# Kernel tuning notes

Hardware: AMD Instinct MI355X
Metric: run time of the kernel (lower is better)

## Reference

```python
import jax, jax.numpy as jnp
import numpy as np

N_STU, N_ITEM, N_CONC = 10000, 50000, 2048
EDGES, K = 250000, 4
EMB, CNUM = 64, 128


def setup_inputs() -> dict:
    key = jax.random.key(0)
    ks = jax.random.split(key, 10)
    return {
        "stu_idx": jax.random.randint(ks[0], (EDGES,), 0, N_STU),
        "item_idx": jax.random.randint(ks[1], (EDGES,), 0, N_ITEM),
        "conc_idx": jax.random.randint(ks[2], (EDGES, K), 0, N_CONC),
        "stu_fusion": jax.random.normal(ks[3], (N_STU, EMB), jnp.float32),
        "item_fusion": jax.random.normal(ks[4], (N_ITEM, EMB), jnp.float32),
        "concept_fusion": jax.random.normal(ks[5], (N_CONC, EMB), jnp.float32),
        # factor weights are non-negative in the original (NoneNegClipper)
        "W_stu": jax.random.uniform(ks[6], (CNUM, 2 * EMB), jnp.float32) * 0.1,
        "W_item": jax.random.uniform(ks[7], (CNUM, 2 * EMB), jnp.float32) * 0.1,
        "w_pred": jax.random.uniform(ks[8], (CNUM,), jnp.float32) * 0.1,
        "b_pred": jax.random.normal(ks[9], (1,), jnp.float32),
    }


def reference(stu_idx, item_idx, conc_idx, stu_fusion, item_fusion,
              concept_fusion, W_stu, W_item, w_pred, b_pred):
    emb = stu_fusion.shape[1]
    # split Linear(2*emb -> CNUM) into the two cat halves: out = x1 @ Wa.T + x2 @ Wb.T
    Ws_a, Ws_b = W_stu[:, :emb], W_stu[:, emb:]
    Wi_a, Wi_b = W_item[:, :emb], W_item[:, emb:]

    # per-entity projections computed once on the tables, then gathered (cheap)
    stu_part = (stu_fusion @ Ws_a.T)[stu_idx]      # [E, CNUM]
    item_part = (item_fusion @ Wi_a.T)[item_idx]   # [E, CNUM]
    conc_stu = (concept_fusion @ Ws_b.T)[conc_idx]   # [E, K, CNUM]
    conc_item = (concept_fusion @ Wi_b.T)[conc_idx]  # [E, K, CNUM]

    stu_out = jax.nn.sigmoid(stu_part[:, None, :] + conc_stu)    # [E, K, CNUM]
    item_out = jax.nn.sigmoid(item_part[:, None, :] + conc_item)  # [E, K, CNUM]
    diff = stu_out - item_out
    per_conc = jax.nn.sigmoid(jnp.einsum('ekc,c->ek', diff, w_pred) + b_pred[0])  # [E, K]
    return per_conc.mean(axis=1)  # [E]
```

## Files before the change

kernel.cpp:

```cpp
#include <hip/hip_runtime.h>
#include <hip/hip_bf16.h>
#include <hip/hip_fp16.h>

constexpr int EDGES = 250000;
constexpr int EMB   = 64;
constexpr int CNUM  = 128;
constexpr int NSTU  = 10000;
constexpr int NITEM = 50000;
constexpr int NCONC = 2048;

constexpr size_t ESP_OFF = 0;
constexpr size_t EIP_OFF = ESP_OFF + (size_t)NSTU  * CNUM;
constexpr size_t ECS_OFF = EIP_OFF + (size_t)NITEM * CNUM;
constexpr size_t ECI_OFF = ECS_OFF + (size_t)NCONC * CNUM;

constexpr int TILE = 16;
constexpr int STU_TILES   = NSTU  / TILE;
constexpr int ITEM_TILES  = NITEM / TILE;
constexpr int CONC_GROUPS = (NCONC / TILE)*2;
constexpr int TOTAL_BLKS  = STU_TILES + ITEM_TILES + CONC_GROUPS;

constexpr float NEG_LOG2E = -1.44269504088896340736f;

__global__ __launch_bounds__(256) void proj_all(
        const float* __restrict__ stuF, const float* __restrict__ itemF,
        const float* __restrict__ concF,
        const float* __restrict__ W_stu, const float* __restrict__ W_item,
        __half* __restrict__ ESP, __half* __restrict__ EIP,
        __half* __restrict__ ECS, __half* __restrict__ ECI) {
    __shared__ float fs[TILE * EMB];
    const int b    = blockIdx.x;
    const int tid  = threadIdx.x;
    const int wv   = tid >> 6;
    const int lane = tid & 63;
    const int cl   = lane & 31;
    const int kh   = lane >> 5;
    const int c    = wv * 32 + cl;

    const float* F; const float* W; __half* O; int row0, wcol;
    if (b < STU_TILES) {
        F = stuF;  W = W_stu;  O = ESP; row0 = b * TILE; wcol = 0;
    } else if (b < STU_TILES + ITEM_TILES) {
        F = itemF; W = W_item; O = EIP; row0 = (b - STU_TILES) * TILE; wcol = 0;
    } else {
        const int g = b - STU_TILES - ITEM_TILES;
        F = concF; W = (g & 1) ? W_item : W_stu; O = (g & 1) ? ECI : ECS;
        row0 = (g >> 1) * TILE; wcol = EMB;
    }

    ((float4*)fs)[tid] = ((const float4*)(F + (size_t)row0 * EMB))[tid];

    float w[32];
    const float4* Wr = (const float4*)(W + c * (2 * EMB) + wcol + kh * 32);
#pragma unroll
    for (int j = 0; j < 8; ++j) {
        float4 u = Wr[j];
        w[4*j+0] = u.x; w[4*j+1] = u.y; w[4*j+2] = u.z; w[4*j+3] = u.w;
    }
    __syncthreads();

#pragma unroll
    for (int r = 0; r < TILE; ++r) {
        const float4* fr = (const float4*)(fs + r * EMB + kh * 32);
        float a0 = 0.f, a1 = 0.f, a2 = 0.f, a3 = 0.f;
#pragma unroll
        for (int j = 0; j < 8; ++j) {
            float4 u = fr[j];
            a0 = fmaf(u.x, w[4*j+0], a0);
            a1 = fmaf(u.y, w[4*j+1], a1);
            a2 = fmaf(u.z, w[4*j+2], a2);
            a3 = fmaf(u.w, w[4*j+3], a3);
        }
        float d = (a0 + a1) + (a2 + a3);
        d += __shfl_xor(d, 32, 64);
        const float e = __builtin_amdgcn_exp2f(d * NEG_LOG2E);
        if (kh == 0) O[(size_t)(row0 + r) * CNUM + c] = __float2half(e);
    }
}

__device__ __forceinline__ void h8f(const uint4 u, float* f) {
    const __half2* h = (const __half2*)&u;
#pragma unroll
    for (int i = 0; i < 4; ++i) {
        float2 v = __half22float2(h[i]);
        f[2*i] = v.x; f[2*i+1] = v.y;
    }
}

__device__ __forceinline__ float chan(float es, float ec, float ei, float ecc,
                                      float w) {
    const float t = es * ec;
    const float u = ei * ecc;
    return (w * (u - t)) * __builtin_amdgcn_rcpf((1.f + t) * (1.f + u));
}

__device__ __forceinline__ float sigm(float x) {
    return __builtin_amdgcn_rcpf(1.f + __builtin_amdgcn_exp2f(x * NEG_LOG2E));
}

__global__ __launch_bounds__(256) void edge_kernel(
        const int*  __restrict__ stu_idx,
        const int*  __restrict__ item_idx,
        const int4* __restrict__ conc_idx,
        const __half* __restrict__ ESP,
        const __half* __restrict__ EIP,
        const __half* __restrict__ ECS,
        const __half* __restrict__ ECI,
        const float* __restrict__ w_pred,
        const float* __restrict__ b_pred,
        float* __restrict__ out) {
    const int lane = threadIdx.x & 63;
    const int wvg  = (blockIdx.x * blockDim.x + threadIdx.x) >> 6;
    const int sub  = lane >> 4;
    const int li   = lane & 15;
    const int e    = wvg * 4 + sub;

    const int s  = stu_idx[e];
    const int it = item_idx[e];
    const int4 c4 = conc_idx[e];

    float es[8], ei[8], wf[8];
    h8f(*(const uint4*)(ESP + (size_t)s  * CNUM + li * 8), es);
    h8f(*(const uint4*)(EIP + (size_t)it * CNUM + li * 8), ei);
    {
        const float4* wp4 = (const float4*)(w_pred + li * 8);
        float4 a = wp4[0], b4 = wp4[1];
        wf[0]=a.x; wf[1]=a.y; wf[2]=a.z; wf[3]=a.w;
        wf[4]=b4.x; wf[5]=b4.y; wf[6]=b4.z; wf[7]=b4.w;
    }
    const float b = b_pred[0];

    const int ck[4] = {c4.x, c4.y, c4.z, c4.w};
    float p[4];
#pragma unroll
    for (int k = 0; k < 4; ++k) {
        float cs[8], ci[8];
        h8f(*(const uint4*)(ECS + (size_t)ck[k] * CNUM + li * 8), cs);
        h8f(*(const uint4*)(ECI + (size_t)ck[k] * CNUM + li * 8), ci);
        float a0 = 0.f, a1 = 0.f;
#pragma unroll
        for (int j = 0; j < 8; j += 2) {
            a0 += chan(es[j],   cs[j],   ei[j],   ci[j],   wf[j]);
            a1 += chan(es[j+1], cs[j+1], ei[j+1], ci[j+1], wf[j+1]);
        }
        p[k] = a0 + a1;
    }

#pragma unroll
    for (int m = 1; m <= 8; m <<= 1) {
        p[0] += __shfl_xor(p[0], m, 64);
        p[1] += __shfl_xor(p[1], m, 64);
        p[2] += __shfl_xor(p[2], m, 64);
        p[3] += __shfl_xor(p[3], m, 64);
    }

    const float r = 0.25f * (sigm(p[0] + b) + sigm(p[1] + b) +
                             sigm(p[2] + b) + sigm(p[3] + b));
    if (li == 0) out[e] = r;
}

extern "C" void kernel_launch(void* const* d_in, const int* in_sizes, int n_in,
                              void* d_out, int out_size, void* d_ws, size_t ws_size,
                              hipStream_t stream) {
    const int* stu_idx  = (const int*)d_in[0];
    const int* item_idx = (const int*)d_in[1];
    const int* conc_idx = (const int*)d_in[2];
    const float* stu_fusion     = (const float*)d_in[3];
    const float* item_fusion    = (const float*)d_in[4];
    const float* concept_fusion = (const float*)d_in[5];
    const float* W_stu          = (const float*)d_in[6];
    const float* W_item         = (const float*)d_in[7];
    const float* w_pred         = (const float*)d_in[8];
    const float* b_pred         = (const float*)d_in[9];
    float* out = (float*)d_out;

    __half* ESP = (__half*)d_ws + ESP_OFF;
    __half* EIP = (__half*)d_ws + EIP_OFF;
    __half* ECS = (__half*)d_ws + ECS_OFF;
    __half* ECI = (__half*)d_ws + ECI_OFF;

    proj_all<<<TOTAL_BLKS, 256, 0, stream>>>(
        stu_fusion, item_fusion, concept_fusion, W_stu, W_item,
        ESP, EIP, ECS, ECI);

    edge_kernel<<<EDGES / 16, 256, 0, stream>>>(
        stu_idx, item_idx, (const int4*)conc_idx,
        ESP, EIP, ECS, ECI, w_pred, b_pred, out);
}
```

Measured before the change: 150.8 us.

## Compute table projections with fp16 MFMA, one 16-row strip per wavefront

Replaces the scalar-FMA projection kernel with a per-wavefront MFMA 16x16x32 fp16 matrix multiply. Each wave handles one 16-row strip across all 128 channels, converting the fp32 features and weights to fp16 in registers. The goal is to cut the ALU-bound projection cost and the LDS staging. In exchange it adds fp16 rounding of inputs before accumulation, and the weights are reloaded from global memory by every wave.

```diff
diff --git a/kernel.cpp b/kernel.cpp
--- a/kernel.cpp
+++ b/kernel.cpp
@@ -14,67 +14,77 @@
 constexpr size_t ECS_OFF = EIP_OFF + (size_t)NITEM * CNUM;
 constexpr size_t ECI_OFF = ECS_OFF + (size_t)NCONC * CNUM;
 
-constexpr int TILE = 16;
-constexpr int STU_TILES   = NSTU  / TILE;
-constexpr int ITEM_TILES  = NITEM / TILE;
-constexpr int CONC_GROUPS = (NCONC / TILE)*2;
-constexpr int TOTAL_BLKS  = STU_TILES + ITEM_TILES + CONC_GROUPS;
-
 constexpr float NEG_LOG2E = -1.44269504088896340736f;
 
-__global__ __launch_bounds__(256) void proj_all(
+constexpr int STU_JOBS  = NSTU  / 16;
+constexpr int ITEM_JOBS = NITEM / 16;
+constexpr int CONC_JOBS = (NCONC / 16) * 2;
+constexpr int NJOBS     = STU_JOBS + ITEM_JOBS + CONC_JOBS;
+constexpr int PROJ_BLKS = (NJOBS + 3) / 4;
+
+typedef _Float16 half8 __attribute__((ext_vector_type(8)));
+typedef float    f32x4 __attribute__((ext_vector_type(4)));
+
+__device__ __forceinline__ half8 pack8(float4 lo, float4 hi) {
+    half8 h;
+    h[0] = (_Float16)lo.x; h[1] = (_Float16)lo.y;
+    h[2] = (_Float16)lo.z; h[3] = (_Float16)lo.w;
+    h[4] = (_Float16)hi.x; h[5] = (_Float16)hi.y;
+    h[6] = (_Float16)hi.z; h[7] = (_Float16)hi.w;
+    return h;
+}
+
+__global__ __launch_bounds__(256) void proj_mfma(
         const float* __restrict__ stuF, const float* __restrict__ itemF,
         const float* __restrict__ concF,
         const float* __restrict__ W_stu, const float* __restrict__ W_item,
         __half* __restrict__ ESP, __half* __restrict__ EIP,
         __half* __restrict__ ECS, __half* __restrict__ ECI) {
-    __shared__ float fs[TILE * EMB];
-    const int b    = blockIdx.x;
     const int tid  = threadIdx.x;
-    const int wv   = tid >> 6;
     const int lane = tid & 63;
-    const int cl   = lane & 31;
-    const int kh   = lane >> 5;
-    const int c    = wv * 32 + cl;
+    const int job  = blockIdx.x * 4 + (tid >> 6);
+    if (job >= NJOBS) return;
 
-    const float* F; const float* W; __half* O; int row0, wcol;
-    if (b < STU_TILES) {
-        F = stuF;  W = W_stu;  O = ESP; row0 = b * TILE; wcol = 0;
-    } else if (b < STU_TILES + ITEM_TILES) {
-        F = itemF; W = W_item; O = EIP; row0 = (b - STU_TILES) * TILE; wcol = 0;
+    const float* F; const float* W; __half* O; int strip, wcol;
+    if (job < STU_JOBS) {
+        F = stuF;  W = W_stu;  O = ESP; strip = job; wcol = 0;
+    } else if (job < STU_JOBS + ITEM_JOBS) {
+        F = itemF; W = W_item; O = EIP; strip = job - STU_JOBS; wcol = 0;
     } else {
-        const int g = b - STU_TILES - ITEM_TILES;
+        const int g = job - STU_JOBS - ITEM_JOBS;
         F = concF; W = (g & 1) ? W_item : W_stu; O = (g & 1) ? ECI : ECS;
-        row0 = (g >> 1) * TILE; wcol = EMB;
+        strip = g >> 1; wcol = EMB;
     }
 
-    ((float4*)fs)[tid] = ((const float4*)(F + (size_t)row0 * EMB))[tid];
+    const int m = lane & 15;
+    const int q = lane >> 4;
+    const int row = strip * 16 + m;
 
-    float w[32];
-    const float4* Wr = (const float4*)(W + c * (2 * EMB) + wcol + kh * 32);
-#pragma unroll
-    for (int j = 0; j < 8; ++j) {
-        float4 u = Wr[j];
-        w[4*j+0] = u.x; w[4*j+1] = u.y; w[4*j+2] = u.z; w[4*j+3] = u.w;
-    }
-    __syncthreads();
+    const float4* fa = (const float4*)(F + (size_t)row * EMB + q * 8);
+    const float4* fb = (const float4*)(F + (size_t)row * EMB + 32 + q * 8);
+    const half8 A0 = pack8(fa[0], fa[1]);
+    const half8 A1 = pack8(fb[0], fb[1]);
+
+    const int orow = strip * 16 + q * 4;
 
 #pragma unroll
-    for (int r = 0; r < TILE; ++r) {
-        const float4* fr = (const float4*)(fs + r * EMB + kh * 32);
-        float a0 = 0.f, a1 = 0.f, a2 = 0.f, a3 = 0.f;
+    for (int ct = 0; ct < 8; ++ct) {
+        const int ch = ct * 16 + m;
+        const float* wr = W + (size_t)ch * (2 * EMB) + wcol;
+        const float4* wb0 = (const float4*)(wr + q * 8);
+        const float4* wb1 = (const float4*)(wr + 32 + q * 8);
+        const half8 B0 = pack8(wb0[0], wb0[1]);
+        const half8 B1 = pack8(wb1[0], wb1[1]);
+
+        f32x4 acc = {0.f, 0.f, 0.f, 0.f};
+        acc = __builtin_amdgcn_mfma_f32_16x16x32_f16(A0, B0, acc, 0, 0, 0);
+        acc = __builtin_amdgcn_mfma_f32_16x16x32_f16(A1, B1, acc, 0, 0, 0);
+
 #pragma unroll
-        for (int j = 0; j < 8; ++j) {
-            float4 u = fr[j];
-            a0 = fmaf(u.x, w[4*j+0], a0);
-            a1 = fmaf(u.y, w[4*j+1], a1);
-            a2 = fmaf(u.z, w[4*j+2], a2);
-            a3 = fmaf(u.w, w[4*j+3], a3);
+        for (int r = 0; r < 4; ++r) {
+            const float e = __builtin_amdgcn_exp2f(acc[r] * NEG_LOG2E);
+            O[(size_t)(orow + r) * CNUM + ct * 16 + m] = __float2half(e);
         }
-        float d = (a0 + a1) + (a2 + a3);
-        d += __shfl_xor(d, 32, 64);
-        const float e = __builtin_amdgcn_exp2f(d * NEG_LOG2E);
-        if (kh == 0) O[(size_t)(row0 + r) * CNUM + c] = __float2half(e);
     }
 }
 
@@ -179,7 +189,7 @@
     __half* ECS = (__half*)d_ws + ECS_OFF;
     __half* ECI = (__half*)d_ws + ECI_OFF;
 
-    proj_all<<<TOTAL_BLKS, 256, 0, stream>>>(
+    proj_mfma<<<PROJ_BLKS, 256, 0, stream>>>(
         stu_fusion, item_fusion, concept_fusion, W_stu, W_item,
         ESP, EIP, ECS, ECI);
 
```

Measured after the change: 145.2 us. 3.7% less time.
